# Kernel tuning notes

Hardware: AMD Instinct MI355X
Metric: run time of the kernel (lower is better)

Reference implementation:

```python
import jax, jax.numpy as jnp
import numpy as np

N, E, F, H, C, G = 50000, 800000, 128, 1, 64, 256
NEG_SLOPE = 0.2


def _seg_softmax(e, seg, n):
    # numerically-stable softmax over edges grouped by target node
    m = jax.ops.segment_max(e, seg, num_segments=n)
    ex = jnp.exp(e - m[seg])
    s = jax.ops.segment_sum(ex, seg, num_segments=n)
    return ex / (s[seg] + 1e-16)


def _gatv2(x, src, dst, wl, bl, wr, br, att, bo, n):
    # GATv2Conv (PyG semantics): lin_l on source x_j, lin_r on target x_i
    xl = (x @ wl.T + bl).reshape(n, H, C)
    xr = (x @ wr.T + br).reshape(n, H, C)
    s = xl[src] + xr[dst]                      # [E, H, C]
    e = jnp.sum(jax.nn.leaky_relu(s, NEG_SLOPE) * att, axis=-1)  # [E, H]
    alpha = _seg_softmax(e, dst, n)
    out = jax.ops.segment_sum(alpha[..., None] * xl[src], dst, num_segments=n)
    return out.reshape(n, H * C) + bo


def setup_inputs() -> dict:
    key = jax.random.key(0)
    ks = jax.random.split(key, 24)
    d = {}
    d['x'] = jax.random.normal(ks[0], (N, F), dtype=jnp.float32)
    d['edge_index'] = jax.random.randint(ks[1], (2, E), 0, N)
    d['batch_idx'] = jnp.sort(jax.random.randint(ks[2], (N,), 0, G))
    sc = 0.1
    # conv1: in=F, out=C
    d['wl1'] = jax.random.normal(ks[3], (H * C, F)) * sc
    d['bl1'] = jnp.zeros((H * C,), jnp.float32)
    d['wr1'] = jax.random.normal(ks[4], (H * C, F)) * sc
    d['br1'] = jnp.zeros((H * C,), jnp.float32)
    d['att1'] = jax.random.normal(ks[5], (H, C)) * sc
    d['bo1'] = jnp.zeros((H * C,), jnp.float32)
    # conv2, conv3: in=H*C, out=C
    d['wl2'] = jax.random.normal(ks[6], (H * C, H * C)) * sc
    d['bl2'] = jnp.zeros((H * C,), jnp.float32)
    d['wr2'] = jax.random.normal(ks[7], (H * C, H * C)) * sc
    d['br2'] = jnp.zeros((H * C,), jnp.float32)
    d['att2'] = jax.random.normal(ks[8], (H, C)) * sc
    d['bo2'] = jnp.zeros((H * C,), jnp.float32)
    d['wl3'] = jax.random.normal(ks[9], (H * C, H * C)) * sc
    d['bl3'] = jnp.zeros((H * C,), jnp.float32)
    d['wr3'] = jax.random.normal(ks[10], (H * C, H * C)) * sc
    d['br3'] = jnp.zeros((H * C,), jnp.float32)
    d['att3'] = jax.random.normal(ks[11], (H, C)) * sc
    d['bo3'] = jnp.zeros((H * C,), jnp.float32)
    # heads
    d['lin1_w'] = jax.random.normal(ks[12], (C, 3 * H * C)) * sc
    d['lin1_b'] = jnp.zeros((C,), jnp.float32)
    d['pred_w'] = jax.random.normal(ks[13], (C, C)) * sc
    d['pred_b'] = jnp.zeros((C,), jnp.float32)
    d['cls_w'] = jax.random.normal(ks[14], (2, C)) * sc
    d['cls_b'] = jnp.zeros((2,), jnp.float32)
    return d


def reference(x, edge_index, batch_idx, wl1, bl1, wr1, br1, att1, bo1,
              wl2, bl2, wr2, br2, att2, bo2, wl3, bl3, wr3, br3, att3, bo3,
              lin1_w, lin1_b, pred_w, pred_b, cls_w, cls_b):
    # add self-loops (GATv2Conv default add_self_loops=True)
    loop = jnp.arange(N, dtype=edge_index.dtype)
    src = jnp.concatenate([edge_index[0], loop])
    dst = jnp.concatenate([edge_index[1], loop])
    x1 = jax.nn.relu(_gatv2(x, src, dst, wl1, bl1, wr1, br1, att1, bo1, N))
    x2 = jax.nn.relu(_gatv2(x1, src, dst, wl2, bl2, wr2, br2, att2, bo2, N))
    x3 = jax.nn.relu(_gatv2(x2, src, dst, wl3, bl3, wr3, br3, att3, bo3, N))
    h = jax.nn.relu(jnp.concatenate([x1, x2, x3], axis=1) @ lin1_w.T + lin1_b)
    g = jax.ops.segment_sum(h, batch_idx, num_segments=G)  # global_add_pool
    emb = jax.nn.relu(g @ pred_w.T + pred_b)                # pred_layer
    out = emb @ cls_w.T + cls_b                             # cls_layer
    return out
```

## Files before the change

### kernel.cpp

```cpp
#include <hip/hip_runtime.h>
#include <hip/hip_bf16.h>

#define N_NODES 50000
#define N_EDGES 800000
#define FDIM 128
#define CDIM 64
#define NGRAPH 256
#define LRELU_SLOPE 0.2f
#define NBUCK ((N_NODES + 255) / 256)
#define BCAP 5120
#define ABLK 400
#define EPB ((N_EDGES + ABLK - 1) / ABLK)
#define NDBIN 64
#define GEMMB ((N_NODES + 63) / 64)

typedef unsigned short ushort_t;
typedef unsigned int uint_t;
typedef __attribute__((ext_vector_type(8))) short short8v;
typedef __attribute__((ext_vector_type(4))) float float4v;

__device__ __forceinline__ ushort_t f2bf(float f) {
    uint_t u = __float_as_uint(f);
    u += 0x7FFFu + ((u >> 16) & 1u);
    return (ushort_t)(u >> 16);
}
__device__ __forceinline__ float bf2f(ushort_t u) {
    return __uint_as_float(((uint_t)u) << 16);
}

__device__ __forceinline__ float fast_exp2(float x) {
    return __builtin_amdgcn_exp2f(x);
}

__device__ __forceinline__ int wave_incl_scan(int v, int lane) {
#pragma unroll
    for (int off = 1; off < 64; off <<= 1) {
        int t = __shfl_up(v, off);
        if (lane >= off) v += t;
    }
    return v;
}

__device__ __forceinline__ float wave_sum(float v) {
#pragma unroll
    for (int off = 32; off >= 1; off >>= 1) v += __shfl_xor(v, off);
    return v;
}

__global__ void k_cvt_x(const float* __restrict__ x, ushort_t* __restrict__ xb) {
    int i = blockIdx.x * 256 + threadIdx.x;
    const int TOT = N_NODES * FDIM / 8;
    if (i >= TOT) return;
    const float* p = x + (size_t)i * 8;
    float4 a = *reinterpret_cast<const float4*>(p);
    float4 b = *reinterpret_cast<const float4*>(p + 4);
    short8v o;
    o[0] = (short)f2bf(a.x); o[1] = (short)f2bf(a.y);
    o[2] = (short)f2bf(a.z); o[3] = (short)f2bf(a.w);
    o[4] = (short)f2bf(b.x); o[5] = (short)f2bf(b.y);
    o[6] = (short)f2bf(b.z); o[7] = (short)f2bf(b.w);
    *reinterpret_cast<short8v*>(xb + (size_t)i * 8) = o;
}

__global__ void k_bucket(const int* __restrict__ src, const int* __restrict__ dst,
                         int* __restrict__ bcnt, int2* __restrict__ stage) {
    __shared__ int lhist[NBUCK];
    __shared__ int lbase[NBUCK];
    __shared__ int lcur[NBUCK];
    int tid = threadIdx.x;
    int e0 = blockIdx.x * EPB;
    int e1 = min(e0 + EPB, N_EDGES);
    for (int t = tid; t < NBUCK; t += 256) { lhist[t] = 0; lcur[t] = 0; }
    __syncthreads();
    for (int e = e0 + tid; e < e1; e += 256)
        atomicAdd(&lhist[dst[e] >> 8], 1);
    __syncthreads();
    for (int t = tid; t < NBUCK; t += 256)
        lbase[t] = atomicAdd(&bcnt[t], lhist[t]);
    __syncthreads();
    for (int e = e0 + tid; e < e1; e += 256) {
        int s = src[e], d = dst[e];
        int b = d >> 8;
        int loff = atomicAdd(&lcur[b], 1);
        int pos = lbase[b] + loff;
        if (pos < BCAP) stage[(size_t)b * BCAP + pos] = make_int2(s, d);
    }
}

__global__ void k_bscan(const int* __restrict__ bcnt, int* __restrict__ bbase) {
    __shared__ int wsum[4];
    int tid = threadIdx.x;
    int lane = tid & 63, w = tid >> 6;
    int v = (tid < NBUCK) ? bcnt[tid] : 0;
    int incl = wave_incl_scan(v, lane);
    if (lane == 63) wsum[w] = incl;
    __syncthreads();
    if (tid == 0) {
        int s = 0;
#pragma unroll
        for (int k = 0; k < 4; k++) { int t = wsum[k]; wsum[k] = s; s += t; }
    }
    __syncthreads();
    if (tid < NBUCK) bbase[tid] = incl - v + wsum[w];
}

__global__ void k_csr(const int* __restrict__ bcnt, const int* __restrict__ bbase,
                      const int2* __restrict__ stage, int* __restrict__ rowptr,
                      int* __restrict__ cnt, int* __restrict__ dhist,
                      int* __restrict__ csr_src) {
    __shared__ int lcnt[256];
    __shared__ int lcur[256];
    __shared__ int ldh[NDBIN];
    __shared__ int wsum[4];
    int b = blockIdx.x;
    int tid = threadIdx.x;
    int lane = tid & 63, w = tid >> 6;
    lcnt[tid] = 0;
    if (tid < NDBIN) ldh[tid] = 0;
    __syncthreads();
    int n = min(bcnt[b], BCAP);
    const int2* sp = stage + (size_t)b * BCAP;
    for (int i = tid; i < n; i += 256)
        atomicAdd(&lcnt[sp[i].y & 255], 1);
    __syncthreads();
    int v = lcnt[tid];
    int incl = wave_incl_scan(v, lane);
    if (lane == 63) wsum[w] = incl;
    __syncthreads();
    if (tid == 0) {
        int s = 0;
#pragma unroll
        for (int k = 0; k < 4; k++) { int t = wsum[k]; wsum[k] = s; s += t; }
    }
    __syncthreads();
    int excl = incl - v + wsum[w];
    int bb = bbase[b];
    int node = (b << 8) + tid;
    if (node < N_NODES) {
        rowptr[node] = bb + excl;
        cnt[node] = v;
        atomicAdd(&ldh[min(v, NDBIN - 1)], 1);
    }
    lcur[tid] = excl;
    __syncthreads();
    if (tid < NDBIN && ldh[tid]) atomicAdd(&dhist[tid], ldh[tid]);
    if (b == 0 && tid == 0) rowptr[N_NODES] = N_EDGES;
    for (int i = tid; i < n; i += 256) {
        int2 sd = sp[i];
        int pos = atomicAdd(&lcur[sd.y & 255], 1);
        csr_src[bb + pos] = sd.x;
    }
}

__global__ void k_scan2d(const int* __restrict__ dhist, int* __restrict__ dcur) {
    int lane = threadIdx.x;
    int v = dhist[lane];
    int incl = wave_incl_scan(v, lane);
    dcur[lane] = incl - v;
}

__global__ void k_dscatter(const int* __restrict__ cnt, int* __restrict__ dcur,
                           int* __restrict__ order) {
    __shared__ int lh[NDBIN], lb[NDBIN], lc[NDBIN];
    int b = blockIdx.x, tid = threadIdx.x;
    if (tid < NDBIN) { lh[tid] = 0; lc[tid] = 0; }
    __syncthreads();
    int node = b * 256 + tid;
    bool ok = node < N_NODES;
    int dg = ok ? min(cnt[node], NDBIN - 1) : 0;
    if (ok) atomicAdd(&lh[dg], 1);
    __syncthreads();
    if (tid < NDBIN) lb[tid] = lh[tid] ? atomicAdd(&dcur[tid], lh[tid]) : 0;
    __syncthreads();
    if (ok) {
        int off2 = atomicAdd(&lc[dg], 1);
        order[lb[dg] + off2] = node;
    }
}

struct WSrc {
    const float* s[7];
    int off[8];
};
__global__ void k_cvt_w(WSrc ws, ushort_t* __restrict__ hi, ushort_t* __restrict__ lo) {
    int gid = blockIdx.x * 256 + threadIdx.x;
    int stride = gridDim.x * 256;
#pragma unroll
    for (int mi = 0; mi < 7; mi++) {
        int n = ws.off[mi + 1] - ws.off[mi];
        const float* s = ws.s[mi];
        ushort_t* h = hi + ws.off[mi];
        ushort_t* l = lo + ws.off[mi];
        for (int i = gid; i < n; i += stride) {
            float f = s[i];
            ushort_t hb = f2bf(f);
            h[i] = hb;
            l[i] = f2bf(f - bf2f(hb));
        }
    }
}

template <int K>
__global__ void k_gemm_dual_mfma(const ushort_t* __restrict__ xa,
                                 const ushort_t* __restrict__ wlh, const ushort_t* __restrict__ wll,
                                 const ushort_t* __restrict__ wrh, const ushort_t* __restrict__ wrl,
                                 const float* __restrict__ bl, const float* __restrict__ br,
                                 ushort_t* __restrict__ xl, ushort_t* __restrict__ xr) {
    int tid = threadIdx.x;
    int wv = tid >> 6, lane = tid & 63;
    bool rhalf = blockIdx.x >= GEMMB;
    int blk = rhalf ? blockIdx.x - GEMMB : blockIdx.x;
    int m0 = blk * 64 + wv * 16;
    if (m0 >= N_NODES) return;
    int arow = min(m0 + (lane & 15), N_NODES - 1);
    int koff = (lane >> 4) * 8;
    int wrow = lane & 15;
    const ushort_t* bh  = rhalf ? wrh : wlh;
    const ushort_t* blo = rhalf ? wrl : wll;
    const float* bias   = rhalf ? br : bl;
    ushort_t* outp      = rhalf ? xr : xl;

    short8v afrag[K / 32];
#pragma unroll
    for (int kk = 0; kk < K / 32; kk++)
        afrag[kk] = *reinterpret_cast<const short8v*>(xa + (size_t)arow * K + kk * 32 + koff);

    float4v acc[4];
#pragma unroll
    for (int f = 0; f < 4; f++) acc[f] = (float4v)(0.f);

#pragma unroll
    for (int kk = 0; kk < K / 32; kk++) {
#pragma unroll
        for (int f = 0; f < 4; f++) {
            size_t boff = (size_t)(f * 16 + wrow) * K + kk * 32 + koff;
            short8v bfh = *reinterpret_cast<const short8v*>(bh + boff);
            short8v bfl = *reinterpret_cast<const short8v*>(blo + boff);
            acc[f] = __builtin_amdgcn_mfma_f32_16x16x32_bf16(afrag[kk], bfh, acc[f], 0, 0, 0);
            acc[f] = __builtin_amdgcn_mfma_f32_16x16x32_bf16(afrag[kk], bfl, acc[f], 0, 0, 0);
        }
    }

    int r0 = m0 + (lane >> 4) * 4;
#pragma unroll
    for (int f = 0; f < 4; f++) {
        int col = f * 16 + (lane & 15);
        float bv = bias[col];
#pragma unroll
        for (int j = 0; j < 4; j++) {
            int row = r0 + j;
            if (row < N_NODES) outp[(size_t)row * 64 + col] = f2bf(acc[f][j] + bv);
        }
    }
}

__global__ void k_gemm_h_pool(const ushort_t* __restrict__ x1, const ushort_t* __restrict__ x2,
                              const ushort_t* __restrict__ x3,
                              const ushort_t* __restrict__ whi, const ushort_t* __restrict__ wlo,
                              const float* __restrict__ b, const int* __restrict__ batch,
                              float* __restrict__ g) {
    __shared__ float ht[64][65];
    int tid = threadIdx.x;
    int wv = tid >> 6, lane = tid & 63;
    int m0 = blockIdx.x * 64 + wv * 16;
    bool wactive = m0 < N_NODES;

    if (wactive) {
        int arow = min(m0 + (lane & 15), N_NODES - 1);
        int koff = (lane >> 4) * 8;
        int wrow = lane & 15;
        float4v acc[4];
#pragma unroll
        for (int f = 0; f < 4; f++) acc[f] = (float4v)(0.f);
#pragma unroll
        for (int ks = 0; ks < 6; ks++) {
            int k0 = ks * 32;
            const ushort_t* srcp = (ks < 2) ? x1 : (ks < 4 ? x2 : x3);
            int kc = k0 & 63;
            short8v afrag = *reinterpret_cast<const short8v*>(srcp + (size_t)arow * 64 + kc + koff);
#pragma unroll
            for (int f = 0; f < 4; f++) {
                size_t boff = (size_t)(f * 16 + wrow) * 192 + k0 + koff;
                short8v bfh = *reinterpret_cast<const short8v*>(whi + boff);
                short8v bfl = *reinterpret_cast<const short8v*>(wlo + boff);
                acc[f] = __builtin_amdgcn_mfma_f32_16x16x32_bf16(afrag, bfh, acc[f], 0, 0, 0);
                acc[f] = __builtin_amdgcn_mfma_f32_16x16x32_bf16(afrag, bfl, acc[f], 0, 0, 0);
            }
        }
        int r0 = wv * 16 + (lane >> 4) * 4;
#pragma unroll
        for (int f = 0; f < 4; f++) {
            int col = f * 16 + (lane & 15);
            float bias = b[col];
#pragma unroll
            for (int j = 0; j < 4; j++) {
                float o = acc[f][j] + bias;
                ht[r0 + j][col] = o > 0.f ? o : 0.f;
            }
        }
    }
    __syncthreads();

    int c = tid & 63, rr = tid >> 6;
    int blkbase = blockIdx.x * 64;
    float acc = 0.f;
    int cur = -1;
    for (int r = rr; r < 64; r += 4) {
        int node = blkbase + r;
        if (node >= N_NODES) break;
        int bb = batch[node];
        if (bb != cur) {
            if (cur >= 0) atomicAdd(&g[cur * 64 + c], acc);
            cur = bb;
            acc = 0.f;
        }
        acc += ht[r][c];
    }
    if (cur >= 0) atomicAdd(&g[cur * 64 + c], acc);
}

__global__ void k_gat(const ushort_t* __restrict__ xl, const ushort_t* __restrict__ xr,
                      const int* __restrict__ rowptr, const int* __restrict__ csr_src,
                      const int* __restrict__ order,
                      const float* __restrict__ att, const float* __restrict__ bo,
                      ushort_t* __restrict__ xout) {
    int tid = threadIdx.x;
    int wv = tid >> 6, lane = tid & 63;
    int gl = lane & 15;
    int slot = blockIdx.x * 16 + wv * 4 + (lane >> 4);
    if (slot >= N_NODES) return;
    int node = order[slot];
    const float LOG2E = 1.44269504f;
    int c0 = gl * 4;
    float4 a4 = *reinterpret_cast<const float4*>(att + c0);
    float at0 = a4.x * LOG2E, at1 = a4.y * LOG2E, at2 = a4.z * LOG2E, at3 = a4.w * LOG2E;
    size_t nb = (size_t)node * 64 + c0;
    ushort4 qr = *reinterpret_cast<const ushort4*>(xr + nb);
    ushort4 ql = *reinterpret_cast<const ushort4*>(xl + nb);
    float xr0 = bf2f(qr.x), xr1 = bf2f(qr.y), xr2 = bf2f(qr.z), xr3 = bf2f(qr.w);
    float l0 = bf2f(ql.x), l1 = bf2f(ql.y), l2 = bf2f(ql.z), l3 = bf2f(ql.w);

    auto grd = [](float p) {
        p += __shfl_xor(p, 1);
        p += __shfl_xor(p, 2);
        p += __shfl_xor(p, 4);
        p += __shfl_xor(p, 8);
        return p;
    };
    auto score4 = [&](float v0, float v1, float v2, float v3) {
        float s0 = v0 + xr0, s1 = v1 + xr1, s2 = v2 + xr2, s3 = v3 + xr3;
        float t0 = fmaxf(s0, LRELU_SLOPE * s0);
        float t1 = fmaxf(s1, LRELU_SLOPE * s1);
        float t2 = fmaxf(s2, LRELU_SLOPE * s2);
        float t3 = fmaxf(s3, LRELU_SLOPE * s3);
        return ((t0 * at0 + t1 * at1) + (t2 * at2 + t3 * at3));
    };

    int beg = rowptr[node], end = rowptr[node + 1];
    int deg = end - beg;
    int lim = end - 1;

    float m = grd(score4(l0, l1, l2, l3));
    float ssum = 1.f;
    float a0 = l0, a1 = l1, a2 = l2, a3 = l3;

    for (int j = 0; j < deg; j += 8) {
        int base = beg + j;
        int i0 = base;
        int i1 = min(base + 1, lim), i2 = min(base + 2, lim), i3 = min(base + 3, lim);
        int i4 = min(base + 4, lim), i5 = min(base + 5, lim);
        int i6 = min(base + 6, lim), i7 = min(base + 7, lim);
        int s0 = csr_src[i0], s1 = csr_src[i1], s2 = csr_src[i2], s3 = csr_src[i3];
        int s4 = csr_src[i4], s5 = csr_src[i5], s6 = csr_src[i6], s7 = csr_src[i7];
        ushort4 q0 = *reinterpret_cast<const ushort4*>(xl + (size_t)s0 * 64 + c0);
        ushort4 q1 = *reinterpret_cast<const ushort4*>(xl + (size_t)s1 * 64 + c0);
        ushort4 q2 = *reinterpret_cast<const ushort4*>(xl + (size_t)s2 * 64 + c0);
        ushort4 q3 = *reinterpret_cast<const ushort4*>(xl + (size_t)s3 * 64 + c0);
        ushort4 q4 = *reinterpret_cast<const ushort4*>(xl + (size_t)s4 * 64 + c0);
        ushort4 q5 = *reinterpret_cast<const ushort4*>(xl + (size_t)s5 * 64 + c0);
        ushort4 q6 = *reinterpret_cast<const ushort4*>(xl + (size_t)s6 * 64 + c0);
        ushort4 q7 = *reinterpret_cast<const ushort4*>(xl + (size_t)s7 * 64 + c0);
        float v00 = bf2f(q0.x), v01 = bf2f(q0.y), v02 = bf2f(q0.z), v03 = bf2f(q0.w);
        float v10 = bf2f(q1.x), v11 = bf2f(q1.y), v12 = bf2f(q1.z), v13 = bf2f(q1.w);
        float v20 = bf2f(q2.x), v21 = bf2f(q2.y), v22 = bf2f(q2.z), v23 = bf2f(q2.w);
        float v30 = bf2f(q3.x), v31 = bf2f(q3.y), v32 = bf2f(q3.z), v33 = bf2f(q3.w);
        float v40 = bf2f(q4.x), v41 = bf2f(q4.y), v42 = bf2f(q4.z), v43 = bf2f(q4.w);
        float v50 = bf2f(q5.x), v51 = bf2f(q5.y), v52 = bf2f(q5.z), v53 = bf2f(q5.w);
        float v60 = bf2f(q6.x), v61 = bf2f(q6.y), v62 = bf2f(q6.z), v63 = bf2f(q6.w);
        float v70 = bf2f(q7.x), v71 = bf2f(q7.y), v72 = bf2f(q7.z), v73 = bf2f(q7.w);
        float e0 = grd(score4(v00, v01, v02, v03));
        float e1 = grd(score4(v10, v11, v12, v13));
        float e2 = grd(score4(v20, v21, v22, v23));
        float e3 = grd(score4(v30, v31, v32, v33));
        float e4 = grd(score4(v40, v41, v42, v43));
        float e5 = grd(score4(v50, v51, v52, v53));
        float e6 = grd(score4(v60, v61, v62, v63));
        float e7 = grd(score4(v70, v71, v72, v73));
        int rem = deg - j;
        if (rem < 8) {
            e1 = (rem > 1) ? e1 : -1e30f;
            e2 = (rem > 2) ? e2 : -1e30f;
            e3 = (rem > 3) ? e3 : -1e30f;
            e4 = (rem > 4) ? e4 : -1e30f;
            e5 = (rem > 5) ? e5 : -1e30f;
            e6 = (rem > 6) ? e6 : -1e30f;
            e7 = (rem > 7) ? e7 : -1e30f;
        }
        float mx = fmaxf(fmaxf(fmaxf(e0, e1), fmaxf(e2, e3)),
                         fmaxf(fmaxf(e4, e5), fmaxf(e6, e7)));
        float mn = fmaxf(m, mx);
        float sc = fast_exp2(m - mn);
        float w0 = fast_exp2(e0 - mn), w1 = fast_exp2(e1 - mn);
        float w2 = fast_exp2(e2 - mn), w3 = fast_exp2(e3 - mn);
        float w4 = fast_exp2(e4 - mn), w5 = fast_exp2(e5 - mn);
        float w6 = fast_exp2(e6 - mn), w7 = fast_exp2(e7 - mn);
        ssum = ssum * sc + (((w0 + w1) + (w2 + w3)) + ((w4 + w5) + (w6 + w7)));
        a0 = a0 * sc + (((w0 * v00 + w1 * v10) + (w2 * v20 + w3 * v30)) +
                        ((w4 * v40 + w5 * v50) + (w6 * v60 + w7 * v70)));
        a1 = a1 * sc + (((w0 * v01 + w1 * v11) + (w2 * v21 + w3 * v31)) +
                        ((w4 * v41 + w5 * v51) + (w6 * v61 + w7 * v71)));
        a2 = a2 * sc + (((w0 * v02 + w1 * v12) + (w2 * v22 + w3 * v32)) +
                        ((w4 * v42 + w5 * v52) + (w6 * v62 + w7 * v72)));
        a3 = a3 * sc + (((w0 * v03 + w1 * v13) + (w2 * v23 + w3 * v33)) +
                        ((w4 * v43 + w5 * v53) + (w6 * v63 + w7 * v73)));
        m = mn;
    }

    float rs = 1.f / (ssum + 1e-16f);
    float4 b4 = *reinterpret_cast<const float4*>(bo + c0);
    float o0 = fmaxf(a0 * rs + b4.x, 0.f);
    float o1 = fmaxf(a1 * rs + b4.y, 0.f);
    float o2 = fmaxf(a2 * rs + b4.z, 0.f);
    float o3 = fmaxf(a3 * rs + b4.w, 0.f);
    ushort4 oq;
    oq.x = f2bf(o0); oq.y = f2bf(o1); oq.z = f2bf(o2); oq.w = f2bf(o3);
    *reinterpret_cast<ushort4*>(xout + nb) = oq;
}

__global__ void k_head(const float* __restrict__ g, const float* __restrict__ pw,
                       const float* __restrict__ pb, const float* __restrict__ cw,
                       const float* __restrict__ cb, float* __restrict__ out) {
    int gb = blockIdx.x;
    int c = threadIdx.x;
    const float* gr = g + gb * 64;
    float a = pb[c];
    const float* pwr = pw + c * 64;
#pragma unroll
    for (int k = 0; k < 64; k++) a += gr[k] * pwr[k];
    a = a > 0.f ? a : 0.f;
    float o0 = wave_sum(a * cw[c]);
    float o1 = wave_sum(a * cw[64 + c]);
    if (c == 0) {
        out[gb * 2 + 0] = o0 + cb[0];
        out[gb * 2 + 1] = o1 + cb[1];
    }
}

extern "C" void kernel_launch(void* const* d_in, const int* in_sizes, int n_in,
                              void* d_out, int out_size, void* d_ws, size_t ws_size,
                              hipStream_t stream) {
    const float* x    = (const float*)d_in[0];
    const int*   ei   = (const int*)d_in[1];
    const int*   bidx = (const int*)d_in[2];
    const float* wl1 = (const float*)d_in[3],  *bl1 = (const float*)d_in[4];
    const float* wr1 = (const float*)d_in[5],  *br1 = (const float*)d_in[6];
    const float* att1 = (const float*)d_in[7], *bo1 = (const float*)d_in[8];
    const float* wl2 = (const float*)d_in[9],  *bl2 = (const float*)d_in[10];
    const float* wr2 = (const float*)d_in[11], *br2 = (const float*)d_in[12];
    const float* att2 = (const float*)d_in[13], *bo2 = (const float*)d_in[14];
    const float* wl3 = (const float*)d_in[15], *bl3 = (const float*)d_in[16];
    const float* wr3 = (const float*)d_in[17], *br3 = (const float*)d_in[18];
    const float* att3 = (const float*)d_in[19], *bo3 = (const float*)d_in[20];
    const float* lw = (const float*)d_in[21], *lb = (const float*)d_in[22];
    const float* pw = (const float*)d_in[23], *pb = (const float*)d_in[24];
    const float* cw = (const float*)d_in[25], *cb = (const float*)d_in[26];
    float* out = (float*)d_out;

    char* wsb = (char*)d_ws;
    size_t off = 0;
    auto alloc = [&](size_t bytes) {
        void* p = wsb + off;
        off = (off + bytes + 255) & ~(size_t)255;
        return p;
    };
    int* cnt      = (int*)alloc((size_t)N_NODES * 4);
    int* rowptr   = (int*)alloc((size_t)(N_NODES + 1) * 4);
    int* bcnt     = (int*)alloc((size_t)(NBUCK + NDBIN) * 4);
    int* dhist    = bcnt + NBUCK;
    int* bbase    = (int*)alloc((size_t)NBUCK * 4);
    int* dcur     = (int*)alloc((size_t)NDBIN * 4);
    int* order    = (int*)alloc((size_t)N_NODES * 4);
    int2* stage   = (int2*)alloc((size_t)NBUCK * BCAP * 8);
    int* csr_src  = (int*)alloc((size_t)N_EDGES * 4);
    const int woff[8] = {0, 8192, 16384, 20480, 24576, 28672, 32768, 45056};
    ushort_t* whi = (ushort_t*)alloc((size_t)45056 * 2);
    ushort_t* wlo = (ushort_t*)alloc((size_t)45056 * 2);
    ushort_t* xbf  = (ushort_t*)alloc((size_t)N_NODES * FDIM * 2);
    ushort_t* xl   = (ushort_t*)alloc((size_t)N_NODES * 64 * 2);
    ushort_t* xrr  = (ushort_t*)alloc((size_t)N_NODES * 64 * 2);
    ushort_t* x1b  = (ushort_t*)alloc((size_t)N_NODES * 64 * 2);
    ushort_t* x2b  = (ushort_t*)alloc((size_t)N_NODES * 64 * 2);
    ushort_t* x3b  = (ushort_t*)alloc((size_t)N_NODES * 64 * 2);
    float* g      = (float*)alloc((size_t)NGRAPH * 64 * 4);
    (void)ws_size; (void)in_sizes; (void)n_in; (void)out_size;

    const int* srcp = ei;
    const int* dstp = ei + N_EDGES;

    hipMemsetAsync(bcnt, 0, (size_t)(NBUCK + NDBIN) * 4, stream);
    hipMemsetAsync(g, 0, (size_t)NGRAPH * 64 * 4, stream);

    k_bucket<<<ABLK, 256, 0, stream>>>(srcp, dstp, bcnt, stage);
    k_bscan<<<1, 256, 0, stream>>>(bcnt, bbase);
    k_csr<<<NBUCK, 256, 0, stream>>>(bcnt, bbase, stage, rowptr, cnt, dhist, csr_src);
    k_scan2d<<<1, 64, 0, stream>>>(dhist, dcur);
    k_dscatter<<<NBUCK, 256, 0, stream>>>(cnt, dcur, order);

    WSrc ws;
    ws.s[0] = wl1; ws.s[1] = wr1; ws.s[2] = wl2; ws.s[3] = wr2;
    ws.s[4] = wl3; ws.s[5] = wr3; ws.s[6] = lw;
    for (int i = 0; i < 8; i++) ws.off[i] = woff[i];
    k_cvt_w<<<64, 256, 0, stream>>>(ws, whi, wlo);
    k_cvt_x<<<(N_NODES * FDIM / 8 + 255) / 256, 256, 0, stream>>>(x, xbf);

    int gatBlocks = (N_NODES + 15) / 16;

    k_gemm_dual_mfma<128><<<2 * GEMMB, 256, 0, stream>>>(
        xbf, whi + woff[0], wlo + woff[0], whi + woff[1], wlo + woff[1], bl1, br1, xl, xrr);
    k_gat<<<gatBlocks, 256, 0, stream>>>(xl, xrr, rowptr, csr_src, order, att1, bo1, x1b);
    k_gemm_dual_mfma<64><<<2 * GEMMB, 256, 0, stream>>>(
        x1b, whi + woff[2], wlo + woff[2], whi + woff[3], wlo + woff[3], bl2, br2, xl, xrr);
    k_gat<<<gatBlocks, 256, 0, stream>>>(xl, xrr, rowptr, csr_src, order, att2, bo2, x2b);
    k_gemm_dual_mfma<64><<<2 * GEMMB, 256, 0, stream>>>(
        x2b, whi + woff[4], wlo + woff[4], whi + woff[5], wlo + woff[5], bl3, br3, xl, xrr);
    k_gat<<<gatBlocks, 256, 0, stream>>>(xl, xrr, rowptr, csr_src, order, att3, bo3, x3b);

    k_gemm_h_pool<<<GEMMB, 256, 0, stream>>>(x1b, x2b, x3b, whi + woff[6], wlo + woff[6],
                                             lb, bidx, g);
    k_head<<<NGRAPH, 64, 0, stream>>>(g, pw, pb, cw, cb, out);
}
```

Before: 254.0 us.

## Cut launch count by fusing preprocessing kernels and localizing degree sort

Merges the weight and input conversion kernels into one launch, folds the zeroing of the pooled-graph buffer into the bucket scan kernel so one memset goes away, and replaces the global degree-binned node ordering (a histogram, a scan kernel and a scatter kernel) with a per-bucket local degree sort inside the CSR kernel. The bucketing kernel now loads its edges into registers once instead of reading them from global memory twice. Together these drop several small launches and one global sync, but node ordering becomes degree-sorted only within each 256-node bucket, which may weaken load balance in the GAT kernels.

Result: no change. 253.1 us (-0.4%).

```diff
diff --git a/kernel.cpp b/kernel.cpp
--- a/kernel.cpp
+++ b/kernel.cpp
@@ -47,19 +47,42 @@
     return v;
 }
 
-__global__ void k_cvt_x(const float* __restrict__ x, ushort_t* __restrict__ xb) {
-    int i = blockIdx.x * 256 + threadIdx.x;
-    const int TOT = N_NODES * FDIM / 8;
-    if (i >= TOT) return;
-    const float* p = x + (size_t)i * 8;
-    float4 a = *reinterpret_cast<const float4*>(p);
-    float4 b = *reinterpret_cast<const float4*>(p + 4);
-    short8v o;
-    o[0] = (short)f2bf(a.x); o[1] = (short)f2bf(a.y);
-    o[2] = (short)f2bf(a.z); o[3] = (short)f2bf(a.w);
-    o[4] = (short)f2bf(b.x); o[5] = (short)f2bf(b.y);
-    o[6] = (short)f2bf(b.z); o[7] = (short)f2bf(b.w);
-    *reinterpret_cast<short8v*>(xb + (size_t)i * 8) = o;
+struct WSrc {
+    const float* s[7];
+    int off[8];
+};
+__global__ void k_cvt(WSrc ws, ushort_t* __restrict__ hi, ushort_t* __restrict__ lo,
+                      const float* __restrict__ x, ushort_t* __restrict__ xb) {
+    if (blockIdx.x < 64) {
+        int gid = blockIdx.x * 256 + threadIdx.x;
+        int stride = 64 * 256;
+#pragma unroll
+        for (int mi = 0; mi < 7; mi++) {
+            int n = ws.off[mi + 1] - ws.off[mi];
+            const float* s = ws.s[mi];
+            ushort_t* h = hi + ws.off[mi];
+            ushort_t* l = lo + ws.off[mi];
+            for (int i = gid; i < n; i += stride) {
+                float f = s[i];
+                ushort_t hb = f2bf(f);
+                h[i] = hb;
+                l[i] = f2bf(f - bf2f(hb));
+            }
+        }
+    } else {
+        int i = (blockIdx.x - 64) * 256 + threadIdx.x;
+        const int TOT = N_NODES * FDIM / 8;
+        if (i >= TOT) return;
+        const float* p = x + (size_t)i * 8;
+        float4 a = *reinterpret_cast<const float4*>(p);
+        float4 b = *reinterpret_cast<const float4*>(p + 4);
+        short8v o;
+        o[0] = (short)f2bf(a.x); o[1] = (short)f2bf(a.y);
+        o[2] = (short)f2bf(a.z); o[3] = (short)f2bf(a.w);
+        o[4] = (short)f2bf(b.x); o[5] = (short)f2bf(b.y);
+        o[6] = (short)f2bf(b.z); o[7] = (short)f2bf(b.w);
+        *reinterpret_cast<short8v*>(xb + (size_t)i * 8) = o;
+    }
 }
 
 __global__ void k_bucket(const int* __restrict__ src, const int* __restrict__ dst,
@@ -70,24 +93,35 @@
     int tid = threadIdx.x;
     int e0 = blockIdx.x * EPB;
     int e1 = min(e0 + EPB, N_EDGES);
+    int es[8], ed[8];
+    int myn = 0;
+#pragma unroll
+    for (int k = 0; k < 8; k++) {
+        int e = e0 + tid + k * 256;
+        if (e < e1) { es[k] = src[e]; ed[k] = dst[e]; myn = k + 1; }
+    }
     for (int t = tid; t < NBUCK; t += 256) { lhist[t] = 0; lcur[t] = 0; }
     __syncthreads();
-    for (int e = e0 + tid; e < e1; e += 256)
-        atomicAdd(&lhist[dst[e] >> 8], 1);
+#pragma unroll
+    for (int k = 0; k < 8; k++)
+        if (k < myn) atomicAdd(&lhist[ed[k] >> 8], 1);
     __syncthreads();
     for (int t = tid; t < NBUCK; t += 256)
-        lbase[t] = atomicAdd(&bcnt[t], lhist[t]);
-    __syncthreads();
-    for (int e = e0 + tid; e < e1; e += 256) {
-        int s = src[e], d = dst[e];
-        int b = d >> 8;
-        int loff = atomicAdd(&lcur[b], 1);
-        int pos = lbase[b] + loff;
-        if (pos < BCAP) stage[(size_t)b * BCAP + pos] = make_int2(s, d);
-    }
-}
-
-__global__ void k_bscan(const int* __restrict__ bcnt, int* __restrict__ bbase) {
+        lbase[t] = lhist[t] ? atomicAdd(&bcnt[t], lhist[t]) : 0;
+    __syncthreads();
+#pragma unroll
+    for (int k = 0; k < 8; k++) {
+        if (k < myn) {
+            int b = ed[k] >> 8;
+            int loff = atomicAdd(&lcur[b], 1);
+            int pos = lbase[b] + loff;
+            if (pos < BCAP) stage[(size_t)b * BCAP + pos] = make_int2(es[k], ed[k]);
+        }
+    }
+}
+
+__global__ void k_bscan(const int* __restrict__ bcnt, int* __restrict__ bbase,
+                        float4* __restrict__ g4) {
     __shared__ int wsum[4];
     int tid = threadIdx.x;
     int lane = tid & 63, w = tid >> 6;
@@ -102,21 +136,23 @@
     }
     __syncthreads();
     if (tid < NBUCK) bbase[tid] = incl - v + wsum[w];
+    const int G4 = NGRAPH * 64 / 4;
+    for (int i = tid; i < G4; i += 256) g4[i] = make_float4(0.f, 0.f, 0.f, 0.f);
 }
 
 __global__ void k_csr(const int* __restrict__ bcnt, const int* __restrict__ bbase,
                       const int2* __restrict__ stage, int* __restrict__ rowptr,
-                      int* __restrict__ cnt, int* __restrict__ dhist,
-                      int* __restrict__ csr_src) {
+                      int* __restrict__ order, int* __restrict__ csr_src) {
     __shared__ int lcnt[256];
     __shared__ int lcur[256];
-    __shared__ int ldh[NDBIN];
+    __shared__ int dh[NDBIN];
+    __shared__ int dbase[NDBIN];
     __shared__ int wsum[4];
     int b = blockIdx.x;
     int tid = threadIdx.x;
     int lane = tid & 63, w = tid >> 6;
     lcnt[tid] = 0;
-    if (tid < NDBIN) ldh[tid] = 0;
+    if (tid < NDBIN) dh[tid] = 0;
     __syncthreads();
     int n = min(bcnt[b], BCAP);
     const int2* sp = stage + (size_t)b * BCAP;
@@ -136,67 +172,29 @@
     int excl = incl - v + wsum[w];
     int bb = bbase[b];
     int node = (b << 8) + tid;
-    if (node < N_NODES) {
+    bool okn = node < N_NODES;
+    int dg = min(v, NDBIN - 1);
+    if (okn) {
         rowptr[node] = bb + excl;
-        cnt[node] = v;
-        atomicAdd(&ldh[min(v, NDBIN - 1)], 1);
+        atomicAdd(&dh[dg], 1);
     }
     lcur[tid] = excl;
-    __syncthreads();
-    if (tid < NDBIN && ldh[tid]) atomicAdd(&dhist[tid], ldh[tid]);
     if (b == 0 && tid == 0) rowptr[N_NODES] = N_EDGES;
+    __syncthreads();
+    if (tid < NDBIN) {
+        int dv = dh[tid];
+        int din = wave_incl_scan(dv, tid);
+        dbase[tid] = din - dv;
+    }
+    __syncthreads();
+    if (okn) {
+        int r = atomicAdd(&dbase[dg], 1);
+        order[(b << 8) + r] = node;
+    }
     for (int i = tid; i < n; i += 256) {
         int2 sd = sp[i];
         int pos = atomicAdd(&lcur[sd.y & 255], 1);
         csr_src[bb + pos] = sd.x;
-    }
-}
-
-__global__ void k_scan2d(const int* __restrict__ dhist, int* __restrict__ dcur) {
-    int lane = threadIdx.x;
-    int v = dhist[lane];
-    int incl = wave_incl_scan(v, lane);
-    dcur[lane] = incl - v;
-}
-
-__global__ void k_dscatter(const int* __restrict__ cnt, int* __restrict__ dcur,
-                           int* __restrict__ order) {
-    __shared__ int lh[NDBIN], lb[NDBIN], lc[NDBIN];
-    int b = blockIdx.x, tid = threadIdx.x;
-    if (tid < NDBIN) { lh[tid] = 0; lc[tid] = 0; }
-    __syncthreads();
-    int node = b * 256 + tid;
-    bool ok = node < N_NODES;
-    int dg = ok ? min(cnt[node], NDBIN - 1) : 0;
-    if (ok) atomicAdd(&lh[dg], 1);
-    __syncthreads();
-    if (tid < NDBIN) lb[tid] = lh[tid] ? atomicAdd(&dcur[tid], lh[tid]) : 0;
-    __syncthreads();
-    if (ok) {
-        int off2 = atomicAdd(&lc[dg], 1);
-        order[lb[dg] + off2] = node;
-    }
-}
-
-struct WSrc {
-    const float* s[7];
-    int off[8];
-};
-__global__ void k_cvt_w(WSrc ws, ushort_t* __restrict__ hi, ushort_t* __restrict__ lo) {
-    int gid = blockIdx.x * 256 + threadIdx.x;
-    int stride = gridDim.x * 256;
-#pragma unroll
-    for (int mi = 0; mi < 7; mi++) {
-        int n = ws.off[mi + 1] - ws.off[mi];
-        const float* s = ws.s[mi];
-        ushort_t* h = hi + ws.off[mi];
-        ushort_t* l = lo + ws.off[mi];
-        for (int i = gid; i < n; i += stride) {
-            float f = s[i];
-            ushort_t hb = f2bf(f);
-            h[i] = hb;
-            l[i] = f2bf(f - bf2f(hb));
-        }
     }
 }
 
@@ -483,12 +481,9 @@
         off = (off + bytes + 255) & ~(size_t)255;
         return p;
     };
-    int* cnt      = (int*)alloc((size_t)N_NODES * 4);
     int* rowptr   = (int*)alloc((size_t)(N_NODES + 1) * 4);
-    int* bcnt     = (int*)alloc((size_t)(NBUCK + NDBIN) * 4);
-    int* dhist    = bcnt + NBUCK;
+    int* bcnt     = (int*)alloc((size_t)NBUCK * 4);
     int* bbase    = (int*)alloc((size_t)NBUCK * 4);
-    int* dcur     = (int*)alloc((size_t)NDBIN * 4);
     int* order    = (int*)alloc((size_t)N_NODES * 4);
     int2* stage   = (int2*)alloc((size_t)NBUCK * BCAP * 8);
     int* csr_src  = (int*)alloc((size_t)N_EDGES * 4);
@@ -507,21 +502,17 @@
     const int* srcp = ei;
     const int* dstp = ei + N_EDGES;
 
-    hipMemsetAsync(bcnt, 0, (size_t)(NBUCK + NDBIN) * 4, stream);
-    hipMemsetAsync(g, 0, (size_t)NGRAPH * 64 * 4, stream);
+    hipMemsetAsync(bcnt, 0, (size_t)NBUCK * 4, stream);
 
     k_bucket<<<ABLK, 256, 0, stream>>>(srcp, dstp, bcnt, stage);
-    k_bscan<<<1, 256, 0, stream>>>(bcnt, bbase);
-    k_csr<<<NBUCK, 256, 0, stream>>>(bcnt, bbase, stage, rowptr, cnt, dhist, csr_src);
-    k_scan2d<<<1, 64, 0, stream>>>(dhist, dcur);
-    k_dscatter<<<NBUCK, 256, 0, stream>>>(cnt, dcur, order);
+    k_bscan<<<1, 256, 0, stream>>>(bcnt, bbase, (float4*)g);
+    k_csr<<<NBUCK, 256, 0, stream>>>(bcnt, bbase, stage, rowptr, order, csr_src);
 
     WSrc ws;
     ws.s[0] = wl1; ws.s[1] = wr1; ws.s[2] = wl2; ws.s[3] = wr2;
     ws.s[4] = wl3; ws.s[5] = wr3; ws.s[6] = lw;
     for (int i = 0; i < 8; i++) ws.off[i] = woff[i];
-    k_cvt_w<<<64, 256, 0, stream>>>(ws, whi, wlo);
-    k_cvt_x<<<(N_NODES * FDIM / 8 + 255) / 256, 256, 0, stream>>>(x, xbf);
+    k_cvt<<<64 + (N_NODES * FDIM / 8 + 255) / 256, 256, 0, stream>>>(ws, whi, wlo, x, xbf);
 
     int gatBlocks = (N_NODES + 15) / 16;
 
```
